# Performance work log

Measured on AMD Instinct MI355X. Metric: run time of the kernel, lower is better.

## Reference

```python
import jax, jax.numpy as jnp
import numpy as np

N, E, NODE_IN, EDGE_IN, HID, HEADS = 50000, 800000, 64, 32, 64, 2


def setup_inputs() -> dict:
    key = jax.random.key(0)
    ks = jax.random.split(key, 24)
    p = lambda k, shape: (jax.random.normal(k, shape, jnp.float32) * 0.05)
    return {
        "x": jax.random.normal(ks[0], (N, NODE_IN), jnp.float32),
        "edge_index": jax.random.randint(ks[1], (2, E), 0, N),
        "edge_attr": jax.random.normal(ks[2], (E, EDGE_IN), jnp.float32),
        # encoders
        "Wn": p(ks[3], (NODE_IN, HID)), "bn": jnp.zeros((HID,), jnp.float32),
        "We": p(ks[4], (EDGE_IN, HID)), "be": jnp.zeros((HID,), jnp.float32),
        # conv1 (heads=1)
        "W1": p(ks[5], (HID, HID)), "as1": p(ks[6], (1, HID)), "ad1": p(ks[7], (1, HID)),
        "We1": p(ks[8], (HID, HID)), "ae1": p(ks[9], (1, HID)),
        "Wr1": p(ks[10], (HID, HID)), "b1": jnp.zeros((HID,), jnp.float32),
        # conv2 (heads=HEADS)
        "W2": p(ks[11], (HID, HEADS * HID)), "as2": p(ks[12], (HEADS, HID)), "ad2": p(ks[13], (HEADS, HID)),
        "We2": p(ks[14], (HID, HEADS * HID)), "ae2": p(ks[15], (HEADS, HID)),
        "Wr2": p(ks[16], (HID, HEADS * HID)), "b2": jnp.zeros((HEADS * HID,), jnp.float32),
        # output head
        "Wl": p(ks[17], (HEADS * HID, 1)), "bl": jnp.zeros((1,), jnp.float32),
    }


def gat_conv(x, src, dst, eattr, W, a_s, a_d, We_, a_e, Wr, b, heads, num_nodes):
    """PyG GATConv (v1) with edge_dim, add_self_loops(fill='mean'), residual."""
    n_edges = src.shape[0]
    # self-loop edge_attr = scatter-mean of incoming edge attrs per node
    cnt = jax.ops.segment_sum(jnp.ones((n_edges,), x.dtype), dst, num_segments=num_nodes)
    loop_attr = jax.ops.segment_sum(eattr, dst, num_segments=num_nodes) / jnp.maximum(cnt, 1.0)[:, None]
    loop = jnp.arange(num_nodes)
    src = jnp.concatenate([src, loop])
    dst = jnp.concatenate([dst, loop])
    eattr = jnp.concatenate([eattr, loop_attr], axis=0)
    C = W.shape[1] // heads
    h = (x @ W).reshape(num_nodes, heads, C)              # [N,H,C]
    e = (eattr @ We_).reshape(-1, heads, C)               # [E',H,C]
    a_src = jnp.sum(h * a_s, axis=-1)                     # [N,H]
    a_dst = jnp.sum(h * a_d, axis=-1)                     # [N,H]
    a_edge = jnp.sum(e * a_e, axis=-1)                    # [E',H]
    logits = jax.nn.leaky_relu(a_src[src] + a_dst[dst] + a_edge, 0.2)
    m = jax.ops.segment_max(logits, dst, num_segments=num_nodes)
    ex = jnp.exp(logits - m[dst])
    denom = jax.ops.segment_sum(ex, dst, num_segments=num_nodes)
    alpha = ex / (denom[dst] + 1e-16)                     # segment softmax over dst
    out = jax.ops.segment_sum(h[src] * alpha[:, :, None], dst, num_segments=num_nodes)
    return out.reshape(num_nodes, heads * C) + x @ Wr + b


def reference(x, edge_index, edge_attr, Wn, bn, We, be,
              W1, as1, ad1, We1, ae1, Wr1, b1,
              W2, as2, ad2, We2, ae2, Wr2, b2, Wl, bl):
    num_nodes = x.shape[0]
    src, dst = edge_index[0], edge_index[1]
    h = x @ Wn + bn
    ea = edge_attr @ We + be
    h = gat_conv(h, src, dst, ea, W1, as1, ad1, We1, ae1, Wr1, b1, 1, num_nodes)
    h = jax.nn.leaky_relu(h, 0.01)  # dropout inactive (eval)
    h = gat_conv(h, src, dst, ea, W2, as2, ad2, We2, ae2, Wr2, b2, HEADS, num_nodes)
    return (h @ Wl + bl).squeeze(1)  # [N]
```

## Files before the change

### kernel.cpp

```cpp
#include <hip/hip_runtime.h>
#include <hip/hip_bf16.h>
#include <math.h>

#define NODE_IN 64
#define EDGE_IN 32
#define HID 64

__device__ __forceinline__ float leaky02(float x){ return x > 0.f ? x : 0.2f*x; }

__device__ __forceinline__ float wredsum(float v){
  #pragma unroll
  for (int o = 32; o > 0; o >>= 1) v += __shfl_xor(v, o);
  return v;
}
__device__ __forceinline__ float wredmax(float v){
  #pragma unroll
  for (int o = 32; o > 0; o >>= 1) v = fmaxf(v, __shfl_xor(v, o));
  return v;
}

__global__ void k_prep(const float* __restrict__ We,  const float* __restrict__ be,
                       const float* __restrict__ We1, const float* __restrict__ ae1,
                       const float* __restrict__ W2,  const float* __restrict__ as2,
                       const float* __restrict__ ad2, const float* __restrict__ We2,
                       const float* __restrict__ ae2, const float* __restrict__ Wr2,
                       const float* __restrict__ b2,  const float* __restrict__ Wl,
                       const float* __restrict__ bl,  float* __restrict__ wc)
{
  __shared__ float ve1[64], ve2a[64], ve2b[64];
  int k = threadIdx.x;
  if (k < 64) {
    float v1=0.f, va=0.f, vb=0.f, sa0=0.f, sa1=0.f, sd0=0.f, sd1=0.f, t0=0.f, t1=0.f, vr=0.f;
    for (int c = 0; c < 64; c++){
      v1  += We1[k*64+c]     * ae1[c];
      va  += We2[k*128+c]    * ae2[c];
      vb  += We2[k*128+64+c] * ae2[64+c];
      sa0 += W2[k*128+c]     * as2[c];
      sa1 += W2[k*128+64+c]  * as2[64+c];
      sd0 += W2[k*128+c]     * ad2[c];
      sd1 += W2[k*128+64+c]  * ad2[64+c];
      t0  += W2[k*128+c]     * Wl[c];
      t1  += W2[k*128+64+c]  * Wl[64+c];
    }
    for (int j = 0; j < 128; j++) vr += Wr2[k*128+j] * Wl[j];
    ve1[k]=v1; ve2a[k]=va; ve2b[k]=vb;
    wc[128+k]=sa0; wc[192+k]=sa1; wc[256+k]=sd0; wc[320+k]=sd1;
    wc[384+k]=t0;  wc[448+k]=t1;  wc[512+k]=vr;
  }
  __syncthreads();
  if (k < 32) {
    float u1=0.f, ua=0.f, ub=0.f;
    for (int kk = 0; kk < 64; kk++){
      float w = We[k*64+kk];
      u1 += w*ve1[kk]; ua += w*ve2a[kk]; ub += w*ve2b[kk];
    }
    wc[k]=u1; wc[32+k]=ua; wc[64+k]=ub;
  }
  if (k == 0) {
    float c1=0.f, ca=0.f, cb=0.f, co=0.f;
    for (int kk = 0; kk < 64; kk++){ c1+=be[kk]*ve1[kk]; ca+=be[kk]*ve2a[kk]; cb+=be[kk]*ve2b[kk]; }
    for (int j = 0; j < 128; j++) co += b2[j]*Wl[j];
    co += bl[0];
    wc[96]=c1; wc[97]=ca; wc[98]=cb; wc[99]=co;
  }
}

__global__ __launch_bounds__(256) void k_cnt(const int* __restrict__ dst,
                                             int* __restrict__ cnt, int E)
{
  int e = blockIdx.x*256 + threadIdx.x;
  if (e >= E) return;
  atomicAdd(&cnt[dst[e]], 1);
}

__global__ __launch_bounds__(256) void k_scan1(const int* __restrict__ cnt,
                                               int* __restrict__ bsum, int N)
{
  __shared__ int sh[256];
  int b = blockIdx.x, t = threadIdx.x;
  int i0 = b*1024 + t*4;
  int s = 0;
  #pragma unroll
  for (int q = 0; q < 4; q++){ int i = i0+q; if (i < N) s += cnt[i]; }
  sh[t] = s; __syncthreads();
  for (int off = 128; off > 0; off >>= 1){
    if (t < off) sh[t] += sh[t+off];
    __syncthreads();
  }
  if (t == 0) bsum[b] = sh[0];
}

__global__ __launch_bounds__(1024) void k_scan2(int* __restrict__ bsum, int nb,
                                                int* __restrict__ rowptr, int N)
{
  __shared__ int sh[1024];
  int t = threadIdx.x;
  int v = (t < nb) ? bsum[t] : 0;
  sh[t] = v; __syncthreads();
  for (int off = 1; off < 1024; off <<= 1){
    int u = (t >= off) ? sh[t-off] : 0;
    __syncthreads();
    sh[t] += u;
    __syncthreads();
  }
  if (t < nb) bsum[t] = sh[t] - v;
  if (t == nb-1) rowptr[N] = sh[t];
}

__global__ __launch_bounds__(256) void k_scan3(const int* __restrict__ cnt,
    const int* __restrict__ bsum, int* __restrict__ rowptr,
    int* __restrict__ cursor, int N)
{
  __shared__ int sh[256];
  int b = blockIdx.x, t = threadIdx.x;
  int i0 = b*1024 + t*4;
  int c[4]; int s = 0;
  #pragma unroll
  for (int q = 0; q < 4; q++){ int i = i0+q; c[q] = (i < N) ? cnt[i] : 0; s += c[q]; }
  int own = s;
  sh[t] = s; __syncthreads();
  for (int off = 1; off < 256; off <<= 1){
    int u = (t >= off) ? sh[t-off] : 0;
    __syncthreads();
    sh[t] += u;
    __syncthreads();
  }
  int run = bsum[b] + sh[t] - own;
  #pragma unroll
  for (int q = 0; q < 4; q++){
    int i = i0+q;
    if (i < N){ rowptr[i] = run; cursor[i] = run; run += c[q]; }
  }
}

__global__ __launch_bounds__(256) void k_edge_fill(const float* __restrict__ eattr,
    const int* __restrict__ src, const int* __restrict__ dst,
    const float* __restrict__ wc, int* __restrict__ cursor,
    float4* __restrict__ edata, int E)
{
  int e = blockIdx.x*256 + threadIdx.x;
  if (e >= E) return;
  const float4* a4 = (const float4*)(eattr + (size_t)e*EDGE_IN);
  float d1=0.f, da=0.f, db=0.f;
  #pragma unroll
  for (int i = 0; i < 8; i++){
    float4 v = a4[i];
    d1 += v.x*wc[4*i+0]    + v.y*wc[4*i+1]    + v.z*wc[4*i+2]    + v.w*wc[4*i+3];
    da += v.x*wc[32+4*i+0] + v.y*wc[32+4*i+1] + v.z*wc[32+4*i+2] + v.w*wc[32+4*i+3];
    db += v.x*wc[64+4*i+0] + v.y*wc[64+4*i+1] + v.z*wc[64+4*i+2] + v.w*wc[64+4*i+3];
  }
  int d = dst[e];
  int pos = atomicAdd(&cursor[d], 1);
  edata[pos] = make_float4(__int_as_float(src[e]), d1 + wc[96], da + wc[97], db + wc[98]);
}

__global__ __launch_bounds__(256) void k_node(const float* __restrict__ x,
    const float* __restrict__ Wn, const float* __restrict__ bn,
    const float* __restrict__ W1, const float* __restrict__ as1, const float* __restrict__ ad1,
    const float* __restrict__ Wr1, const float* __restrict__ b1,
    float* __restrict__ h1, float* __restrict__ hr1,
    float* __restrict__ asrc1, float* __restrict__ adst1, int N)
{
  __shared__ float sA[128][65];
  __shared__ float sW[64][64];
  __shared__ float sbn[64], sb1[64], sas[64], sad[64];
  int t = threadIdx.x;
  int n0 = blockIdx.x*128;
  int i = t>>2, c0 = (t&3)*16;
  int nA = n0 + i, nB = n0 + 64 + i;

  for (int idx = t; idx < 128*64; idx += 256){
    int r = idx>>6, c = idx&63;
    int node = n0 + r;
    sA[r][c] = (node < N) ? x[(size_t)node*64 + c] : 0.f;
  }
  for (int idx = t; idx < 64*64; idx += 256) sW[idx>>6][idx&63] = Wn[idx];
  if (t < 64){ sbn[t]=bn[t]; sb1[t]=b1[t]; sas[t]=as1[t]; sad[t]=ad1[t]; }
  __syncthreads();

  float hA[16], hB[16];
  #pragma unroll
  for (int cc = 0; cc < 16; cc++){ hA[cc]=0.f; hB[cc]=0.f; }
  for (int k = 0; k < 64; k++){
    float xa = sA[i][k], xb = sA[i+64][k];
    #pragma unroll
    for (int cc = 0; cc < 16; cc++){
      float w = sW[k][c0+cc];
      hA[cc] += xa*w; hB[cc] += xb*w;
    }
  }
  #pragma unroll
  for (int cc = 0; cc < 16; cc++){ hA[cc] += sbn[c0+cc]; hB[cc] += sbn[c0+cc]; }
  #pragma unroll
  for (int cc = 0; cc < 16; cc++){ sA[i][c0+cc] = hA[cc]; sA[i+64][c0+cc] = hB[cc]; }
  __syncthreads();
  for (int idx = t; idx < 64*64; idx += 256) sW[idx>>6][idx&63] = W1[idx];
  __syncthreads();

  float a1A[16], a1B[16];
  #pragma unroll
  for (int cc = 0; cc < 16; cc++){ a1A[cc]=0.f; a1B[cc]=0.f; }
  for (int k = 0; k < 64; k++){
    float ha = sA[i][k], hb = sA[i+64][k];
    #pragma unroll
    for (int cc = 0; cc < 16; cc++){
      float w = sW[k][c0+cc];
      a1A[cc] += ha*w; a1B[cc] += hb*w;
    }
  }
  float psA=0.f, pdA=0.f, psB=0.f, pdB=0.f;
  #pragma unroll
  for (int cc = 0; cc < 16; cc++){
    psA += a1A[cc]*sas[c0+cc]; pdA += a1A[cc]*sad[c0+cc];
    psB += a1B[cc]*sas[c0+cc]; pdB += a1B[cc]*sad[c0+cc];
  }
  psA += __shfl_xor(psA,1); psA += __shfl_xor(psA,2);
  pdA += __shfl_xor(pdA,1); pdA += __shfl_xor(pdA,2);
  psB += __shfl_xor(psB,1); psB += __shfl_xor(psB,2);
  pdB += __shfl_xor(pdB,1); pdB += __shfl_xor(pdB,2);
  if (nA < N){
    #pragma unroll
    for (int q = 0; q < 4; q++)
      *(float4*)&h1[(size_t)nA*64 + c0 + q*4] = make_float4(a1A[q*4],a1A[q*4+1],a1A[q*4+2],a1A[q*4+3]);
    if ((t&3)==0){ asrc1[nA]=psA; adst1[nA]=pdA; }
  }
  if (nB < N){
    #pragma unroll
    for (int q = 0; q < 4; q++)
      *(float4*)&h1[(size_t)nB*64 + c0 + q*4] = make_float4(a1B[q*4],a1B[q*4+1],a1B[q*4+2],a1B[q*4+3]);
    if ((t&3)==0){ asrc1[nB]=psB; adst1[nB]=pdB; }
  }
  __syncthreads();
  for (int idx = t; idx < 64*64; idx += 256) sW[idx>>6][idx&63] = Wr1[idx];
  __syncthreads();

  float arA[16], arB[16];
  #pragma unroll
  for (int cc = 0; cc < 16; cc++){ arA[cc]=0.f; arB[cc]=0.f; }
  for (int k = 0; k < 64; k++){
    float ha = sA[i][k], hb = sA[i+64][k];
    #pragma unroll
    for (int cc = 0; cc < 16; cc++){
      float w = sW[k][c0+cc];
      arA[cc] += ha*w; arB[cc] += hb*w;
    }
  }
  if (nA < N){
    #pragma unroll
    for (int q = 0; q < 4; q++)
      *(float4*)&hr1[(size_t)nA*64 + c0 + q*4] = make_float4(arA[q*4]+sb1[c0+q*4], arA[q*4+1]+sb1[c0+q*4+1],
                                                             arA[q*4+2]+sb1[c0+q*4+2], arA[q*4+3]+sb1[c0+q*4+3]);
  }
  if (nB < N){
    #pragma unroll
    for (int q = 0; q < 4; q++)
      *(float4*)&hr1[(size_t)nB*64 + c0 + q*4] = make_float4(arB[q*4]+sb1[c0+q*4], arB[q*4+1]+sb1[c0+q*4+1],
                                                             arB[q*4+2]+sb1[c0+q*4+2], arB[q*4+3]+sb1[c0+q*4+3]);
  }
}

__global__ __launch_bounds__(256) void k_conv1(const float4* __restrict__ edata,
    const int* __restrict__ rowptr, const float* __restrict__ h1, const float* __restrict__ hr1,
    const float* __restrict__ asrc1, const float* __restrict__ adst1,
    const float* __restrict__ wc, float4* __restrict__ srcvec, float4* __restrict__ nd0,
    float* __restrict__ rres, int N)
{
  int n = (int)((blockIdx.x*blockDim.x + threadIdx.x) >> 6);
  int lane = threadIdx.x & 63;
  if (n >= N) return;
  int base = rowptr[n];
  int deg  = rowptr[n+1] - base;
  float h1n  = h1 [(size_t)n*64 + lane];
  float hr1n = hr1[(size_t)n*64 + lane];
  float adn = adst1[n], asn = asrc1[n];
  float invdeg = deg > 0 ? 1.f/(float)deg : 0.f;

  float acc, ssa, ssb;

  if (deg <= 64){
    bool has = lane < deg;
    float4 ed = has ? edata[base+lane] : make_float4(0.f,0.f,0.f,0.f);
    int s = has ? __float_as_int(ed.x) : n;
    float l = has ? leaky02(asrc1[s] + adn + ed.y) : -1e30f;
    float m = wredmax(l);
    float ss1 = wredsum(ed.y); ssa = wredsum(ed.z); ssb = wredsum(ed.w);
    float ll = leaky02(asn + adn + ss1*invdeg);
    m = fmaxf(m, ll);
    float w = has ? __expf(l - m) : 0.f;
    float den = wredsum(w) + __expf(ll - m);
    float inv = 1.f/(den + 1e-16f);
    w *= inv;

    acc = __expf(ll - m)*inv * h1n;
    for (int kk = 0; kk < deg; kk += 8){
      float ww[8]; int ss[8]; float v[8];
      #pragma unroll
      for (int q = 0; q < 8; q++){ ww[q] = __shfl(w, kk+q); ss[q] = __shfl(s, kk+q); }
      #pragma unroll
      for (int q = 0; q < 8; q++) v[q] = h1[(size_t)ss[q]*64 + lane];
      #pragma unroll
      for (int q = 0; q < 8; q++) acc += ww[q]*v[q];
    }
  } else {
    float m = -1e30f, ss1 = 0.f; ssa = 0.f; ssb = 0.f;
    for (int j = lane; j < deg; j += 64){
      float4 ed = edata[base+j];
      int s = __float_as_int(ed.x);
      float l = leaky02(asrc1[s] + adn + ed.y);
      m = fmaxf(m, l); ss1 += ed.y; ssa += ed.z; ssb += ed.w;
    }
    m = wredmax(m); ss1 = wredsum(ss1); ssa = wredsum(ssa); ssb = wredsum(ssb);
    float ll = leaky02(asn + adn + ss1*invdeg);
    m = fmaxf(m, ll);
    float den = 0.f;
    for (int j = lane; j < deg; j += 64){
      float4 ed = edata[base+j];
      int s = __float_as_int(ed.x);
      den += __expf(leaky02(asrc1[s] + adn + ed.y) - m);
    }
    den = wredsum(den) + __expf(ll - m);
    float inv = 1.f/(den + 1e-16f);
    acc = __expf(ll - m)*inv * h1n;
    for (int cs = 0; cs < deg; cs += 64){
      int j = cs + lane;
      float w = 0.f; int s = n;
      if (j < deg){
        float4 ed = edata[base+j];
        s = __float_as_int(ed.x);
        w = __expf(leaky02(asrc1[s] + adn + ed.y) - m)*inv;
      }
      int kmax = min(64, deg - cs);
      for (int k = 0; k < kmax; k++){
        float wk = __shfl(w, k);
        int   sk = __shfl(s, k);
        acc += wk * h1[(size_t)sk*64 + lane];
      }
    }
  }

  float hAv = acc + hr1n;
  hAv = hAv > 0.f ? hAv : 0.01f*hAv;

  float d0 = wredsum(hAv*wc[128+lane]);
  float d1 = wredsum(hAv*wc[192+lane]);
  float d2 = wredsum(hAv*wc[256+lane]);
  float d3 = wredsum(hAv*wc[320+lane]);
  float d4 = wredsum(hAv*wc[384+lane]);
  float d5 = wredsum(hAv*wc[448+lane]);
  float d6 = wredsum(hAv*wc[512+lane]);
  if (lane == 0){
    srcvec[n] = make_float4(d4, d5, d0, d1);
    nd0[n]    = make_float4(d2, d3, ssa*invdeg, ssb*invdeg);
    rres[n]   = d6;
  }
}

__global__ __launch_bounds__(256) void k_conv2(const float4* __restrict__ edata,
    const int* __restrict__ rowptr, const float4* __restrict__ srcvec,
    const float4* __restrict__ nd0, const float* __restrict__ rres,
    const float* __restrict__ wc, float* __restrict__ out, int N)
{
  int n = (int)((blockIdx.x*blockDim.x + threadIdx.x) >> 6);
  int lane = threadIdx.x & 63;
  if (n >= N) return;
  int base = rowptr[n], deg = rowptr[n+1] - base;
  float4 nd  = nd0[n];
  float4 own = srcvec[n];
  float rn = rres[n];

  float num0, num1, den0, den1, m0, m1;

  if (deg <= 64){
    bool has = lane < deg;
    float4 ed = has ? edata[base+lane] : make_float4(0.f,0.f,0.f,0.f);
    int s = has ? __float_as_int(ed.x) : n;
    float4 sv = srcvec[s];
    float l0 = has ? leaky02(sv.z + nd.x + ed.z) : -1e30f;
    float l1 = has ? leaky02(sv.w + nd.y + ed.w) : -1e30f;
    m0 = wredmax(l0); m1 = wredmax(l1);
    float ll0 = leaky02(own.z + nd.x + nd.z);
    float ll1 = leaky02(own.w + nd.y + nd.w);
    m0 = fmaxf(m0, ll0); m1 = fmaxf(m1, ll1);
    float e0 = has ? __expf(l0 - m0) : 0.f;
    float e1 = has ? __expf(l1 - m1) : 0.f;
    den0 = wredsum(e0); den1 = wredsum(e1);
    num0 = wredsum(e0*sv.x); num1 = wredsum(e1*sv.y);
    float se0 = __expf(ll0 - m0), se1 = __expf(ll1 - m1);
    den0 += se0; den1 += se1; num0 += se0*own.x; num1 += se1*own.y;
  } else {
    m0 = -1e30f; m1 = -1e30f;
    for (int j = lane; j < deg; j += 64){
      float4 ed = edata[base+j];
      int s = __float_as_int(ed.x);
      float4 sv = srcvec[s];
      m0 = fmaxf(m0, leaky02(sv.z + nd.x + ed.z));
      m1 = fmaxf(m1, leaky02(sv.w + nd.y + ed.w));
    }
    m0 = wredmax(m0); m1 = wredmax(m1);
    float ll0 = leaky02(own.z + nd.x + nd.z);
    float ll1 = leaky02(own.w + nd.y + nd.w);
    m0 = fmaxf(m0, ll0); m1 = fmaxf(m1, ll1);
    den0=0.f; den1=0.f; num0=0.f; num1=0.f;
    for (int j = lane; j < deg; j += 64){
      float4 ed = edata[base+j];
      int s = __float_as_int(ed.x);
      float4 sv = srcvec[s];
      float e0 = __expf(leaky02(sv.z + nd.x + ed.z) - m0);
      float e1 = __expf(leaky02(sv.w + nd.y + ed.w) - m1);
      den0 += e0; den1 += e1; num0 += e0*sv.x; num1 += e1*sv.y;
    }
    den0 = wredsum(den0); den1 = wredsum(den1);
    num0 = wredsum(num0); num1 = wredsum(num1);
    float se0 = __expf(ll0 - m0), se1 = __expf(ll1 - m1);
    den0 += se0; den1 += se1; num0 += se0*own.x; num1 += se1*own.y;
  }

  if (lane == 0)
    out[n] = num0/(den0+1e-16f) + num1/(den1+1e-16f) + rn + wc[99];
}

extern "C" void kernel_launch(void* const* d_in, const int* in_sizes, int n_in,
                              void* d_out, int out_size, void* d_ws, size_t ws_size,
                              hipStream_t stream)
{
  const float* x     = (const float*)d_in[0];
  const int*   ei    = (const int*)  d_in[1];
  const float* eattr = (const float*)d_in[2];
  const float* Wn  = (const float*)d_in[3];
  const float* bn  = (const float*)d_in[4];
  const float* We  = (const float*)d_in[5];
  const float* be  = (const float*)d_in[6];
  const float* W1  = (const float*)d_in[7];
  const float* as1 = (const float*)d_in[8];
  const float* ad1 = (const float*)d_in[9];
  const float* We1 = (const float*)d_in[10];
  const float* ae1 = (const float*)d_in[11];
  const float* Wr1 = (const float*)d_in[12];
  const float* b1  = (const float*)d_in[13];
  const float* W2  = (const float*)d_in[14];
  const float* as2 = (const float*)d_in[15];
  const float* ad2 = (const float*)d_in[16];
  const float* We2 = (const float*)d_in[17];
  const float* ae2 = (const float*)d_in[18];
  const float* Wr2 = (const float*)d_in[19];
  const float* b2  = (const float*)d_in[20];
  const float* Wl  = (const float*)d_in[21];
  const float* bl  = (const float*)d_in[22];

  int N = in_sizes[0]/NODE_IN;
  int E = in_sizes[2]/EDGE_IN;
  const int* srcArr = ei;
  const int* dstArr = ei + E;

  char* p = (char*)d_ws;
  auto alloc = [&](size_t bytes)->char* { char* r = p; p += (bytes + 255) & ~(size_t)255; return r; };
  float*  wc     = (float*) alloc(1024*4);
  int*    cnt    = (int*)   alloc((size_t)N*4);
  int*    rowptr = (int*)   alloc((size_t)(N+1)*4);
  int*    cursor = (int*)   alloc((size_t)N*4);
  int*    bsum   = (int*)   alloc(4096*4);
  float4* edata  = (float4*)alloc((size_t)E*16);
  float*  h1     = (float*) alloc((size_t)N*HID*4);
  float*  hr1    = (float*) alloc((size_t)N*HID*4);
  float*  asrc1  = (float*) alloc((size_t)N*4);
  float*  adst1  = (float*) alloc((size_t)N*4);
  float4* srcvec = (float4*)alloc((size_t)N*16);
  float4* nd0    = (float4*)alloc((size_t)N*16);
  float*  rres   = (float*) alloc((size_t)N*4);

  int nb = (N + 1023) / 1024;

  hipMemsetAsync(cnt, 0, (size_t)N*4, stream);
  k_prep<<<1, 64, 0, stream>>>(We, be, We1, ae1, W2, as2, ad2, We2, ae2, Wr2, b2, Wl, bl, wc);
  k_cnt<<<(E+255)/256, 256, 0, stream>>>(dstArr, cnt, E);
  k_scan1<<<nb, 256, 0, stream>>>(cnt, bsum, N);
  k_scan2<<<1, 1024, 0, stream>>>(bsum, nb, rowptr, N);
  k_scan3<<<nb, 256, 0, stream>>>(cnt, bsum, rowptr, cursor, N);
  k_edge_fill<<<(E+255)/256, 256, 0, stream>>>(eattr, srcArr, dstArr, wc, cursor, edata, E);
  k_node<<<(N+127)/128, 256, 0, stream>>>(x, Wn, bn, W1, as1, ad1, Wr1, b1, h1, hr1, asrc1, adst1, N);
  k_conv1<<<(N+3)/4, 256, 0, stream>>>(edata, rowptr, h1, hr1, asrc1, adst1, wc, srcvec, nd0, rres, N);
  k_conv2<<<(N+3)/4, 256, 0, stream>>>(edata, rowptr, srcvec, nd0, rres, wc, (float*)d_out, N);
}
```

Measured before the change: 417.3 us.

## Process one node per 16-lane group with float4 gathers in conv kernels

Both conv kernels now map each node to a 16-lane subgroup instead of a full 64-lane wavefront, with each lane handling four feature channels through float4 loads. Reductions use 4-step shuffles within the group, and the fast path covers degree up to 32 via two edges per lane. The weight-precompute kernel is folded into the edge-count kernel, which now reads four dst indices per thread. This aims to cut idle lanes and shuffle overhead for low-degree nodes (average degree about 16) and to drop one launch, at the cost of more per-lane work and serialised gathers for high-degree nodes.

```diff
diff --git a/kernel.cpp b/kernel.cpp
--- a/kernel.cpp
+++ b/kernel.cpp
@@ -8,69 +8,75 @@
 
 __device__ __forceinline__ float leaky02(float x){ return x > 0.f ? x : 0.2f*x; }
 
-__device__ __forceinline__ float wredsum(float v){
-  #pragma unroll
-  for (int o = 32; o > 0; o >>= 1) v += __shfl_xor(v, o);
+__device__ __forceinline__ float gsum(float v){
+  v += __shfl_xor(v,1); v += __shfl_xor(v,2); v += __shfl_xor(v,4); v += __shfl_xor(v,8);
   return v;
 }
-__device__ __forceinline__ float wredmax(float v){
-  #pragma unroll
-  for (int o = 32; o > 0; o >>= 1) v = fmaxf(v, __shfl_xor(v, o));
+__device__ __forceinline__ float gmax(float v){
+  v = fmaxf(v,__shfl_xor(v,1)); v = fmaxf(v,__shfl_xor(v,2));
+  v = fmaxf(v,__shfl_xor(v,4)); v = fmaxf(v,__shfl_xor(v,8));
   return v;
 }
 
-__global__ void k_prep(const float* __restrict__ We,  const float* __restrict__ be,
-                       const float* __restrict__ We1, const float* __restrict__ ae1,
-                       const float* __restrict__ W2,  const float* __restrict__ as2,
-                       const float* __restrict__ ad2, const float* __restrict__ We2,
-                       const float* __restrict__ ae2, const float* __restrict__ Wr2,
-                       const float* __restrict__ b2,  const float* __restrict__ Wl,
-                       const float* __restrict__ bl,  float* __restrict__ wc)
+__global__ __launch_bounds__(256) void k_cntprep(const int* __restrict__ dst,
+    int* __restrict__ cnt, int E,
+    const float* __restrict__ We,  const float* __restrict__ be,
+    const float* __restrict__ We1, const float* __restrict__ ae1,
+    const float* __restrict__ W2,  const float* __restrict__ as2,
+    const float* __restrict__ ad2, const float* __restrict__ We2,
+    const float* __restrict__ ae2, const float* __restrict__ Wr2,
+    const float* __restrict__ b2,  const float* __restrict__ Wl,
+    const float* __restrict__ bl,  float* __restrict__ wc)
 {
   __shared__ float ve1[64], ve2a[64], ve2b[64];
-  int k = threadIdx.x;
-  if (k < 64) {
-    float v1=0.f, va=0.f, vb=0.f, sa0=0.f, sa1=0.f, sd0=0.f, sd1=0.f, t0=0.f, t1=0.f, vr=0.f;
-    for (int c = 0; c < 64; c++){
-      v1  += We1[k*64+c]     * ae1[c];
-      va  += We2[k*128+c]    * ae2[c];
-      vb  += We2[k*128+64+c] * ae2[64+c];
-      sa0 += W2[k*128+c]     * as2[c];
-      sa1 += W2[k*128+64+c]  * as2[64+c];
-      sd0 += W2[k*128+c]     * ad2[c];
-      sd1 += W2[k*128+64+c]  * ad2[64+c];
-      t0  += W2[k*128+c]     * Wl[c];
-      t1  += W2[k*128+64+c]  * Wl[64+c];
-    }
-    for (int j = 0; j < 128; j++) vr += Wr2[k*128+j] * Wl[j];
-    ve1[k]=v1; ve2a[k]=va; ve2b[k]=vb;
-    wc[128+k]=sa0; wc[192+k]=sa1; wc[256+k]=sd0; wc[320+k]=sd1;
-    wc[384+k]=t0;  wc[448+k]=t1;  wc[512+k]=vr;
-  }
-  __syncthreads();
-  if (k < 32) {
-    float u1=0.f, ua=0.f, ub=0.f;
-    for (int kk = 0; kk < 64; kk++){
-      float w = We[k*64+kk];
-      u1 += w*ve1[kk]; ua += w*ve2a[kk]; ub += w*ve2b[kk];
-    }
-    wc[k]=u1; wc[32+k]=ua; wc[64+k]=ub;
-  }
-  if (k == 0) {
-    float c1=0.f, ca=0.f, cb=0.f, co=0.f;
-    for (int kk = 0; kk < 64; kk++){ c1+=be[kk]*ve1[kk]; ca+=be[kk]*ve2a[kk]; cb+=be[kk]*ve2b[kk]; }
-    for (int j = 0; j < 128; j++) co += b2[j]*Wl[j];
-    co += bl[0];
-    wc[96]=c1; wc[97]=ca; wc[98]=cb; wc[99]=co;
-  }
-}
-
-__global__ __launch_bounds__(256) void k_cnt(const int* __restrict__ dst,
-                                             int* __restrict__ cnt, int E)
-{
-  int e = blockIdx.x*256 + threadIdx.x;
-  if (e >= E) return;
-  atomicAdd(&cnt[dst[e]], 1);
+  int t = threadIdx.x;
+  int i0 = blockIdx.x*1024 + t*4;
+  if (i0 + 3 < E){
+    int4 d = *(const int4*)&dst[i0];
+    atomicAdd(&cnt[d.x],1); atomicAdd(&cnt[d.y],1);
+    atomicAdd(&cnt[d.z],1); atomicAdd(&cnt[d.w],1);
+  } else {
+    #pragma unroll
+    for (int q = 0; q < 4; q++){ int i = i0+q; if (i < E) atomicAdd(&cnt[dst[i]],1); }
+  }
+
+  if (blockIdx.x == gridDim.x - 1){
+    int k = t;
+    if (k < 64) {
+      float v1=0.f, va=0.f, vb=0.f, sa0=0.f, sa1=0.f, sd0=0.f, sd1=0.f, t0=0.f, t1=0.f, vr=0.f;
+      for (int c = 0; c < 64; c++){
+        v1  += We1[k*64+c]     * ae1[c];
+        va  += We2[k*128+c]    * ae2[c];
+        vb  += We2[k*128+64+c] * ae2[64+c];
+        sa0 += W2[k*128+c]     * as2[c];
+        sa1 += W2[k*128+64+c]  * as2[64+c];
+        sd0 += W2[k*128+c]     * ad2[c];
+        sd1 += W2[k*128+64+c]  * ad2[64+c];
+        t0  += W2[k*128+c]     * Wl[c];
+        t1  += W2[k*128+64+c]  * Wl[64+c];
+      }
+      for (int j = 0; j < 128; j++) vr += Wr2[k*128+j] * Wl[j];
+      ve1[k]=v1; ve2a[k]=va; ve2b[k]=vb;
+      wc[128+k]=sa0; wc[192+k]=sa1; wc[256+k]=sd0; wc[320+k]=sd1;
+      wc[384+k]=t0;  wc[448+k]=t1;  wc[512+k]=vr;
+    }
+    __syncthreads();
+    if (k < 32) {
+      float u1=0.f, ua=0.f, ub=0.f;
+      for (int kk = 0; kk < 64; kk++){
+        float w = We[k*64+kk];
+        u1 += w*ve1[kk]; ua += w*ve2a[kk]; ub += w*ve2b[kk];
+      }
+      wc[k]=u1; wc[32+k]=ua; wc[64+k]=ub;
+    }
+    if (k == 0) {
+      float c1=0.f, ca=0.f, cb=0.f, co=0.f;
+      for (int kk = 0; kk < 64; kk++){ c1+=be[kk]*ve1[kk]; ca+=be[kk]*ve2a[kk]; cb+=be[kk]*ve2b[kk]; }
+      for (int j = 0; j < 128; j++) co += b2[j]*Wl[j];
+      co += bl[0];
+      wc[96]=c1; wc[97]=ca; wc[98]=cb; wc[99]=co;
+    }
+  }
 }
 
 __global__ __launch_bounds__(256) void k_scan1(const int* __restrict__ cnt,
@@ -265,93 +271,119 @@
     const float* __restrict__ wc, float4* __restrict__ srcvec, float4* __restrict__ nd0,
     float* __restrict__ rres, int N)
 {
-  int n = (int)((blockIdx.x*blockDim.x + threadIdx.x) >> 6);
-  int lane = threadIdx.x & 63;
+  int tid = blockIdx.x*256 + threadIdx.x;
+  int n = tid >> 4;
+  int sl = threadIdx.x & 15;
+  int gb = threadIdx.x & 48;
   if (n >= N) return;
   int base = rowptr[n];
   int deg  = rowptr[n+1] - base;
-  float h1n  = h1 [(size_t)n*64 + lane];
-  float hr1n = hr1[(size_t)n*64 + lane];
   float adn = adst1[n], asn = asrc1[n];
   float invdeg = deg > 0 ? 1.f/(float)deg : 0.f;
-
-  float acc, ssa, ssb;
-
-  if (deg <= 64){
-    bool has = lane < deg;
-    float4 ed = has ? edata[base+lane] : make_float4(0.f,0.f,0.f,0.f);
-    int s = has ? __float_as_int(ed.x) : n;
-    float l = has ? leaky02(asrc1[s] + adn + ed.y) : -1e30f;
-    float m = wredmax(l);
-    float ss1 = wredsum(ed.y); ssa = wredsum(ed.z); ssb = wredsum(ed.w);
+  float4 h1n4 = *(const float4*)&h1 [(size_t)n*64 + sl*4];
+  float4 hr4  = *(const float4*)&hr1[(size_t)n*64 + sl*4];
+
+  float4 acc;
+  float ssa, ssb;
+
+  if (deg <= 32){
+    bool a0 = sl < deg, a1 = sl+16 < deg;
+    float4 e0 = a0 ? edata[base+sl]    : make_float4(0.f,0.f,0.f,0.f);
+    float4 e1 = a1 ? edata[base+sl+16] : make_float4(0.f,0.f,0.f,0.f);
+    int s0  = a0 ? __float_as_int(e0.x) : n;
+    int s1_ = a1 ? __float_as_int(e1.x) : n;
+    float l0 = a0 ? leaky02(asrc1[s0]  + adn + e0.y) : -1e30f;
+    float l1 = a1 ? leaky02(asrc1[s1_] + adn + e1.y) : -1e30f;
+    float m = gmax(fmaxf(l0,l1));
+    float ss1 = gsum(e0.y + e1.y);
+    ssa = gsum(e0.z + e1.z);
+    ssb = gsum(e0.w + e1.w);
     float ll = leaky02(asn + adn + ss1*invdeg);
     m = fmaxf(m, ll);
-    float w = has ? __expf(l - m) : 0.f;
-    float den = wredsum(w) + __expf(ll - m);
+    float w0 = a0 ? __expf(l0 - m) : 0.f;
+    float w1 = a1 ? __expf(l1 - m) : 0.f;
+    float den = gsum(w0 + w1) + __expf(ll - m);
     float inv = 1.f/(den + 1e-16f);
-    w *= inv;
-
-    acc = __expf(ll - m)*inv * h1n;
-    for (int kk = 0; kk < deg; kk += 8){
-      float ww[8]; int ss[8]; float v[8];
+    w0 *= inv; w1 *= inv;
+    float sw = __expf(ll - m)*inv;
+    acc.x = sw*h1n4.x; acc.y = sw*h1n4.y; acc.z = sw*h1n4.z; acc.w = sw*h1n4.w;
+
+    for (int kk = 0; kk < deg; kk += 4){
+      float wk[4]; int sk[4];
       #pragma unroll
-      for (int q = 0; q < 8; q++){ ww[q] = __shfl(w, kk+q); ss[q] = __shfl(s, kk+q); }
+      for (int q = 0; q < 4; q++){
+        int j = kk + q;
+        float wv = (j < 16) ? w0 : w1;
+        int   svi = (j < 16) ? s0 : s1_;
+        wk[q] = __shfl(wv,  gb + (j & 15));
+        sk[q] = __shfl(svi, gb + (j & 15));
+        if (j >= deg){ wk[q] = 0.f; sk[q] = n; }
+      }
+      float4 v[4];
       #pragma unroll
-      for (int q = 0; q < 8; q++) v[q] = h1[(size_t)ss[q]*64 + lane];
+      for (int q = 0; q < 4; q++) v[q] = *(const float4*)&h1[(size_t)sk[q]*64 + sl*4];
       #pragma unroll
-      for (int q = 0; q < 8; q++) acc += ww[q]*v[q];
+      for (int q = 0; q < 4; q++){
+        acc.x += wk[q]*v[q].x; acc.y += wk[q]*v[q].y;
+        acc.z += wk[q]*v[q].z; acc.w += wk[q]*v[q].w;
+      }
     }
   } else {
-    float m = -1e30f, ss1 = 0.f; ssa = 0.f; ssb = 0.f;
-    for (int j = lane; j < deg; j += 64){
+    float m = -1e30f, ss1 = 0.f, sA_ = 0.f, sB_ = 0.f;
+    for (int j = sl; j < deg; j += 16){
       float4 ed = edata[base+j];
       int s = __float_as_int(ed.x);
-      float l = leaky02(asrc1[s] + adn + ed.y);
-      m = fmaxf(m, l); ss1 += ed.y; ssa += ed.z; ssb += ed.w;
-    }
-    m = wredmax(m); ss1 = wredsum(ss1); ssa = wredsum(ssa); ssb = wredsum(ssb);
+      m = fmaxf(m, leaky02(asrc1[s] + adn + ed.y));
+      ss1 += ed.y; sA_ += ed.z; sB_ += ed.w;
+    }
+    m = gmax(m); ss1 = gsum(ss1); ssa = gsum(sA_); ssb = gsum(sB_);
     float ll = leaky02(asn + adn + ss1*invdeg);
     m = fmaxf(m, ll);
     float den = 0.f;
-    for (int j = lane; j < deg; j += 64){
+    for (int j = sl; j < deg; j += 16){
       float4 ed = edata[base+j];
       int s = __float_as_int(ed.x);
       den += __expf(leaky02(asrc1[s] + adn + ed.y) - m);
     }
-    den = wredsum(den) + __expf(ll - m);
+    den = gsum(den) + __expf(ll - m);
     float inv = 1.f/(den + 1e-16f);
-    acc = __expf(ll - m)*inv * h1n;
-    for (int cs = 0; cs < deg; cs += 64){
-      int j = cs + lane;
+    float sw = __expf(ll - m)*inv;
+    acc.x = sw*h1n4.x; acc.y = sw*h1n4.y; acc.z = sw*h1n4.z; acc.w = sw*h1n4.w;
+    for (int cs = 0; cs < deg; cs += 16){
+      int j = cs + sl;
       float w = 0.f; int s = n;
       if (j < deg){
         float4 ed = edata[base+j];
         s = __float_as_int(ed.x);
         w = __expf(leaky02(asrc1[s] + adn + ed.y) - m)*inv;
       }
-      int kmax = min(64, deg - cs);
+      int kmax = min(16, deg - cs);
       for (int k = 0; k < kmax; k++){
-        float wk = __shfl(w, k);
-        int   sk = __shfl(s, k);
-        acc += wk * h1[(size_t)sk*64 + lane];
+        float wk = __shfl(w, gb + k);
+        int   sk = __shfl(s, gb + k);
+        float4 v = *(const float4*)&h1[(size_t)sk*64 + sl*4];
+        acc.x += wk*v.x; acc.y += wk*v.y; acc.z += wk*v.z; acc.w += wk*v.w;
       }
     }
   }
 
-  float hAv = acc + hr1n;
-  hAv = hAv > 0.f ? hAv : 0.01f*hAv;
-
-  float d0 = wredsum(hAv*wc[128+lane]);
-  float d1 = wredsum(hAv*wc[192+lane]);
-  float d2 = wredsum(hAv*wc[256+lane]);
-  float d3 = wredsum(hAv*wc[320+lane]);
-  float d4 = wredsum(hAv*wc[384+lane]);
-  float d5 = wredsum(hAv*wc[448+lane]);
-  float d6 = wredsum(hAv*wc[512+lane]);
-  if (lane == 0){
-    srcvec[n] = make_float4(d4, d5, d0, d1);
-    nd0[n]    = make_float4(d2, d3, ssa*invdeg, ssb*invdeg);
-    rres[n]   = d6;
+  float4 hv;
+  hv.x = acc.x + hr4.x; hv.y = acc.y + hr4.y; hv.z = acc.z + hr4.z; hv.w = acc.w + hr4.w;
+  hv.x = hv.x > 0.f ? hv.x : 0.01f*hv.x;
+  hv.y = hv.y > 0.f ? hv.y : 0.01f*hv.y;
+  hv.z = hv.z > 0.f ? hv.z : 0.01f*hv.z;
+  hv.w = hv.w > 0.f ? hv.w : 0.01f*hv.w;
+
+  float d[7];
+  #pragma unroll
+  for (int i = 0; i < 7; i++){
+    float4 wv = *(const float4*)&wc[128 + i*64 + sl*4];
+    d[i] = gsum(hv.x*wv.x + hv.y*wv.y + hv.z*wv.z + hv.w*wv.w);
+  }
+  if (sl == 0){
+    srcvec[n] = make_float4(d[4], d[5], d[0], d[1]);
+    nd0[n]    = make_float4(d[2], d[3], ssa*invdeg, ssb*invdeg);
+    rres[n]   = d[6];
   }
 }
 
@@ -360,62 +392,66 @@
     const float4* __restrict__ nd0, const float* __restrict__ rres,
     const float* __restrict__ wc, float* __restrict__ out, int N)
 {
-  int n = (int)((blockIdx.x*blockDim.x + threadIdx.x) >> 6);
-  int lane = threadIdx.x & 63;
+  int tid = blockIdx.x*256 + threadIdx.x;
+  int n = tid >> 4;
+  int sl = threadIdx.x & 15;
   if (n >= N) return;
   int base = rowptr[n], deg = rowptr[n+1] - base;
   float4 nd  = nd0[n];
   float4 own = srcvec[n];
   float rn = rres[n];
-
+  float ll0 = leaky02(own.z + nd.x + nd.z);
+  float ll1 = leaky02(own.w + nd.y + nd.w);
   float num0, num1, den0, den1, m0, m1;
 
-  if (deg <= 64){
-    bool has = lane < deg;
-    float4 ed = has ? edata[base+lane] : make_float4(0.f,0.f,0.f,0.f);
-    int s = has ? __float_as_int(ed.x) : n;
-    float4 sv = srcvec[s];
-    float l0 = has ? leaky02(sv.z + nd.x + ed.z) : -1e30f;
-    float l1 = has ? leaky02(sv.w + nd.y + ed.w) : -1e30f;
-    m0 = wredmax(l0); m1 = wredmax(l1);
-    float ll0 = leaky02(own.z + nd.x + nd.z);
-    float ll1 = leaky02(own.w + nd.y + nd.w);
-    m0 = fmaxf(m0, ll0); m1 = fmaxf(m1, ll1);
-    float e0 = has ? __expf(l0 - m0) : 0.f;
-    float e1 = has ? __expf(l1 - m1) : 0.f;
-    den0 = wredsum(e0); den1 = wredsum(e1);
-    num0 = wredsum(e0*sv.x); num1 = wredsum(e1*sv.y);
-    float se0 = __expf(ll0 - m0), se1 = __expf(ll1 - m1);
-    den0 += se0; den1 += se1; num0 += se0*own.x; num1 += se1*own.y;
+  if (deg <= 32){
+    bool a0 = sl < deg, a1 = sl+16 < deg;
+    float4 e0 = a0 ? edata[base+sl]    : make_float4(0.f,0.f,0.f,0.f);
+    float4 e1 = a1 ? edata[base+sl+16] : make_float4(0.f,0.f,0.f,0.f);
+    int s0  = a0 ? __float_as_int(e0.x) : n;
+    int s1_ = a1 ? __float_as_int(e1.x) : n;
+    float4 sv0 = srcvec[s0];
+    float4 sv1 = srcvec[s1_];
+    float l00 = a0 ? leaky02(sv0.z + nd.x + e0.z) : -1e30f;
+    float l01 = a0 ? leaky02(sv0.w + nd.y + e0.w) : -1e30f;
+    float l10 = a1 ? leaky02(sv1.z + nd.x + e1.z) : -1e30f;
+    float l11 = a1 ? leaky02(sv1.w + nd.y + e1.w) : -1e30f;
+    m0 = gmax(fmaxf(l00,l10)); m0 = fmaxf(m0, ll0);
+    m1 = gmax(fmaxf(l01,l11)); m1 = fmaxf(m1, ll1);
+    float x00 = a0 ? __expf(l00 - m0) : 0.f;
+    float x10 = a1 ? __expf(l10 - m0) : 0.f;
+    float x01 = a0 ? __expf(l01 - m1) : 0.f;
+    float x11 = a1 ? __expf(l11 - m1) : 0.f;
+    den0 = gsum(x00 + x10); den1 = gsum(x01 + x11);
+    num0 = gsum(x00*sv0.x + x10*sv1.x);
+    num1 = gsum(x01*sv0.y + x11*sv1.y);
   } else {
     m0 = -1e30f; m1 = -1e30f;
-    for (int j = lane; j < deg; j += 64){
+    for (int j = sl; j < deg; j += 16){
       float4 ed = edata[base+j];
       int s = __float_as_int(ed.x);
       float4 sv = srcvec[s];
       m0 = fmaxf(m0, leaky02(sv.z + nd.x + ed.z));
       m1 = fmaxf(m1, leaky02(sv.w + nd.y + ed.w));
     }
-    m0 = wredmax(m0); m1 = wredmax(m1);
-    float ll0 = leaky02(own.z + nd.x + nd.z);
-    float ll1 = leaky02(own.w + nd.y + nd.w);
-    m0 = fmaxf(m0, ll0); m1 = fmaxf(m1, ll1);
-    den0=0.f; den1=0.f; num0=0.f; num1=0.f;
-    for (int j = lane; j < deg; j += 64){
+    m0 = gmax(m0); m0 = fmaxf(m0, ll0);
+    m1 = gmax(m1); m1 = fmaxf(m1, ll1);
+    float d0=0.f, d1=0.f, q0=0.f, q1=0.f;
+    for (int j = sl; j < deg; j += 16){
       float4 ed = edata[base+j];
       int s = __float_as_int(ed.x);
       float4 sv = srcvec[s];
-      float e0 = __expf(leaky02(sv.z + nd.x + ed.z) - m0);
-      float e1 = __expf(leaky02(sv.w + nd.y + ed.w) - m1);
-      den0 += e0; den1 += e1; num0 += e0*sv.x; num1 += e1*sv.y;
-    }
-    den0 = wredsum(den0); den1 = wredsum(den1);
-    num0 = wredsum(num0); num1 = wredsum(num1);
-    float se0 = __expf(ll0 - m0), se1 = __expf(ll1 - m1);
-    den0 += se0; den1 += se1; num0 += se0*own.x; num1 += se1*own.y;
-  }
-
-  if (lane == 0)
+      float e0x = __expf(leaky02(sv.z + nd.x + ed.z) - m0);
+      float e1x = __expf(leaky02(sv.w + nd.y + ed.w) - m1);
+      d0 += e0x; d1 += e1x; q0 += e0x*sv.x; q1 += e1x*sv.y;
+    }
+    den0 = gsum(d0); den1 = gsum(d1); num0 = gsum(q0); num1 = gsum(q1);
+  }
+
+  float se0 = __expf(ll0 - m0), se1 = __expf(ll1 - m1);
+  den0 += se0; den1 += se1; num0 += se0*own.x; num1 += se1*own.y;
+
+  if (sl == 0)
     out[n] = num0/(den0+1e-16f) + num1/(den1+1e-16f) + rn + wc[99];
 }
 
@@ -468,16 +504,17 @@
   float4* nd0    = (float4*)alloc((size_t)N*16);
   float*  rres   = (float*) alloc((size_t)N*4);
 
-  int nb = (N + 1023) / 1024;
+  int nbE = (E + 1023) / 1024;
+  int nbN = (N + 1023) / 1024;
 
   hipMemsetAsync(cnt, 0, (size_t)N*4, stream);
-  k_prep<<<1, 64, 0, stream>>>(We, be, We1, ae1, W2, as2, ad2, We2, ae2, Wr2, b2, Wl, bl, wc);
-  k_cnt<<<(E+255)/256, 256, 0, stream>>>(dstArr, cnt, E);
-  k_scan1<<<nb, 256, 0, stream>>>(cnt, bsum, N);
-  k_scan2<<<1, 1024, 0, stream>>>(bsum, nb, rowptr, N);
-  k_scan3<<<nb, 256, 0, stream>>>(cnt, bsum, rowptr, cursor, N);
+  k_cntprep<<<nbE, 256, 0, stream>>>(dstArr, cnt, E,
+      We, be, We1, ae1, W2, as2, ad2, We2, ae2, Wr2, b2, Wl, bl, wc);
+  k_scan1<<<nbN, 256, 0, stream>>>(cnt, bsum, N);
+  k_scan2<<<1, 1024, 0, stream>>>(bsum, nbN, rowptr, N);
+  k_scan3<<<nbN, 256, 0, stream>>>(cnt, bsum, rowptr, cursor, N);
   k_edge_fill<<<(E+255)/256, 256, 0, stream>>>(eattr, srcArr, dstArr, wc, cursor, edata, E);
   k_node<<<(N+127)/128, 256, 0, stream>>>(x, Wn, bn, W1, as1, ad1, Wr1, b1, h1, hr1, asrc1, adst1, N);
-  k_conv1<<<(N+3)/4, 256, 0, stream>>>(edata, rowptr, h1, hr1, asrc1, adst1, wc, srcvec, nd0, rres, N);
-  k_conv2<<<(N+3)/4, 256, 0, stream>>>(edata, rowptr, srcvec, nd0, rres, wc, (float*)d_out, N);
-}
+  k_conv1<<<(N*16+255)/256, 256, 0, stream>>>(edata, rowptr, h1, hr1, asrc1, adst1, wc, srcvec, nd0, rres, N);
+  k_conv2<<<(N*16+255)/256, 256, 0, stream>>>(edata, rowptr, srcvec, nd0, rres, wc, (float*)d_out, N);
+}
```

New measurement: 376.0 us. 1.11x faster.
